# Optimization experiments

Hardware: AMD Instinct MI355X
Metric: run time of the kernel (lower is better)

Reference implementation:

```python
import jax, jax.numpy as jnp
import numpy as np

ND, NT, B = 16384, 16384, 4096
FD, FT, C = 256, 256, 768


def _gat(x_src, x_dst, ei, Ws, Wd, a_s, a_d, b, num_dst, self_loops):
    """PyG GATConv, heads=1: per-edge attention softmax over incoming edges."""
    if self_loops:
        loops = jnp.arange(num_dst, dtype=ei.dtype)
        ei = jnp.concatenate([ei, jnp.stack([loops, loops])], axis=1)
    src, dst = ei[0], ei[1]
    hs = x_src @ Ws                                   # [Ns, C]
    hd = x_dst @ Wd                                   # [Ndst, C]
    e = jax.nn.leaky_relu((hs @ a_s)[src] + (hd @ a_d)[dst], 0.2)   # [E]
    m = jax.ops.segment_max(e, dst, num_segments=num_dst)
    p = jnp.exp(e - m[dst])
    s = jax.ops.segment_sum(p, dst, num_segments=num_dst)
    alpha = p / (s[dst] + 1e-16)
    out = jax.ops.segment_sum(hs[src] * alpha[:, None], dst, num_segments=num_dst)
    return out + b


def _l2norm(x):
    n = jnp.linalg.norm(x, axis=1, keepdims=True)
    return x / jnp.maximum(n, 1e-12)


def setup_inputs() -> dict:
    ks = iter(jax.random.split(jax.random.key(0), 64))
    def nrm(shape, fan_in=None):
        s = 1.0 if fan_in is None else (1.0 / fan_in) ** 0.5
        return jax.random.normal(next(ks), shape, jnp.float32) * s
    inp = {}
    inp["x_drug"] = nrm((ND, FD))
    inp["x_target"] = nrm((NT, FT))
    inp["cell_features"] = nrm((B, 890))
    for et, fs, fd in (("dd", FD, FD), ("dt", FD, FT), ("tt", FT, FT)):
        inp[f"W_src_{et}"] = nrm((fs, C), fs)
        inp[f"W_dst_{et}"] = nrm((fd, C), fd)
        inp[f"a_src_{et}"] = nrm((C,), C)
        inp[f"a_dst_{et}"] = nrm((C,), C)
        inp[f"b_{et}"] = jnp.zeros((C,), jnp.float32)
    for name, fi, fo in (("red1", 890, 2048), ("red2", 2048, 512), ("red3", 512, 2 * C),
                         ("r2a", 4 * C, 2048), ("r2b", 2048, 512), ("r2c", 512, C), ("cls", C, 2)):
        inp[f"{name}_w"] = nrm((fi, fo), fi)
        inp[f"{name}_b"] = jnp.zeros((fo,), jnp.float32)
    inp["drug1_id"] = jax.random.randint(next(ks), (B,), 0, ND)
    inp["drug2_id"] = jax.random.randint(next(ks), (B,), 0, ND)
    inp["ei_dd"] = jax.random.randint(next(ks), (2, 131072), 0, ND)
    inp["ei_dt"] = jnp.stack([jax.random.randint(next(ks), (262144,), 0, ND),
                              jax.random.randint(next(ks), (262144,), 0, NT)])
    inp["ei_tt"] = jax.random.randint(next(ks), (2, 262144), 0, NT)
    return inp


def reference(x_drug, x_target, cell_features,
              W_src_dd, W_dst_dd, a_src_dd, a_dst_dd, b_dd,
              W_src_dt, W_dst_dt, a_src_dt, a_dst_dt, b_dt,
              W_src_tt, W_dst_tt, a_src_tt, a_dst_tt, b_tt,
              red1_w, red1_b, red2_w, red2_b, red3_w, red3_b,
              r2a_w, r2a_b, r2b_w, r2b_b, r2c_w, r2c_b,
              cls_w, cls_b,
              drug1_id, drug2_id, ei_dd, ei_dt, ei_tt):
    # HeteroConv (aggr='sum') followed by per-type ReLU, num_layers=1
    drug = jax.nn.relu(_gat(x_drug, x_drug, ei_dd,
                            W_src_dd, W_dst_dd, a_src_dd, a_dst_dd, b_dd, ND, True))
    target = jax.nn.relu(
        _gat(x_drug, x_target, ei_dt, W_src_dt, W_dst_dt, a_src_dt, a_dst_dt, b_dt, NT, False)
        + _gat(x_target, x_target, ei_tt, W_src_tt, W_dst_tt, a_src_tt, a_dst_tt, b_tt, NT, True))
    del target  # with num_layers=1 the target embeddings never feed the output (faithful)
    d1 = drug[drug1_id]
    d2 = drug[drug2_id]
    cell = _l2norm(cell_features)
    cell = jax.nn.relu(cell @ red1_w + red1_b)
    cell = jax.nn.relu(cell @ red2_w + red2_b)
    cell = jax.nn.relu(cell @ red3_w + red3_b)          # [B, 2*C]
    hidden = _l2norm(jnp.concatenate([d1, d2, cell], axis=1))  # [B, 4*C]
    hidden = jax.nn.relu(hidden @ r2a_w + r2a_b)
    hidden = jax.nn.relu(hidden @ r2b_w + r2b_b)
    hidden = jax.nn.relu(hidden @ r2c_w + r2c_b)
    return hidden @ cls_w + cls_b                       # [B, 2]
```

## Files before the change

kernel.cpp:

```cpp
#include <hip/hip_runtime.h>
#include <cstdint>

#define ND 16384
#define BATCH 4096
#define CDIM 768
#define E_DD 131072
#define FD 256

typedef unsigned short u16;
typedef u16 u16x4 __attribute__((ext_vector_type(4)));
typedef u16 u16x8 __attribute__((ext_vector_type(8)));
typedef short s16x8 __attribute__((ext_vector_type(8)));
typedef float f32x4 __attribute__((ext_vector_type(4)));

__device__ __forceinline__ u16 f2bf(float x) {
  union { float f; uint32_t u; } v; v.f = x;
  uint32_t r = v.u + 0x7fffu + ((v.u >> 16) & 1u);
  return (u16)(r >> 16);
}
__device__ __forceinline__ float bf2f(u16 h) {
  union { float f; uint32_t u; } v; v.u = ((uint32_t)h) << 16;
  return v.f;
}
__device__ __forceinline__ uint32_t split2p(float x) {
  u16 h = f2bf(x);
  u16 l = f2bf(x - bf2f(h));
  return ((uint32_t)h << 16) | l;
}

#define KP 40

template <int KS, int OUT_BF16, int RELU, int BIAS, int ASPLIT, int ALO, int BLO>
__global__ __launch_bounds__(256) void mfma_gemm(
    const float* __restrict__ Af,
    const u16* __restrict__ Ahi, const u16* __restrict__ Alo,
    const u16* __restrict__ Bhi, const u16* __restrict__ Blo,
    const float* __restrict__ bias,
    float* __restrict__ Cf, u16* __restrict__ Chi,
    int M, int N, int K) {
  constexpr int MT = 4, NT = 4;
  constexpr int BM = 128, BN = 128;
  constexpr int ASEG = BM / 64;
  constexpr int BSEG = BN / 64;
  constexpr int AARR = ALO ? 2 : 1;
  constexpr int BARR = BLO ? 2 : 1;
  __shared__ __align__(16) u16 As[AARR][BM][KP];
  __shared__ __align__(16) u16 Bs[BARR][BN][KP];

  const int t = threadIdx.x;
  const int bm0 = blockIdx.x * BM, bn0 = blockIdx.y * BN;
  const int wid = t >> 6, lane = t & 63;
  const int quad = lane >> 4, l16 = lane & 15;
  const int wm0 = (wid >> 1) * (MT * 16);
  const int wn0 = (wid & 1) * (NT * 16);

  const int chunk = K / KS;
  const int kbeg = (KS > 1) ? (int)blockIdx.z * chunk : 0;
  const int kend = kbeg + chunk;

  f32x4 acc[MT][NT];
#pragma unroll
  for (int i = 0; i < MT; ++i)
#pragma unroll
    for (int j = 0; j < NT; ++j) acc[i][j] = (f32x4){0.f, 0.f, 0.f, 0.f};

  u16x8 pAh[ASEG], pAl[ASEG], pBh[BSEG], pBl[BSEG];

  auto loadA = [&](int c, int kk) {
    int s = t + 256 * c, row = s >> 2, kq = (s & 3) * 8;
    size_t off = (size_t)(bm0 + row) * K + kk + kq;
    if (ASPLIT) {
      f32x4 v0 = *(const f32x4*)(Af + off);
      f32x4 v1 = *(const f32x4*)(Af + off + 4);
      u16x8 h, l;
#pragma unroll
      for (int e = 0; e < 4; ++e) {
        uint32_t p = split2p(v0[e]);
        h[e] = (u16)(p >> 16); l[e] = (u16)(p & 0xffffu);
        uint32_t q = split2p(v1[e]);
        h[e + 4] = (u16)(q >> 16); l[e + 4] = (u16)(q & 0xffffu);
      }
      pAh[c] = h; pAl[c] = l;
    } else {
      pAh[c] = *(const u16x8*)(Ahi + off);
      if (ALO) pAl[c] = *(const u16x8*)(Alo + off);
    }
  };
  auto loadB = [&](int c, int kk) {
    int s = t + 256 * c, row = s >> 2, kq = (s & 3) * 8;
    size_t off = (size_t)(bn0 + row) * K + kk + kq;
    pBh[c] = *(const u16x8*)(Bhi + off);
    if (BLO) pBl[c] = *(const u16x8*)(Blo + off);
  };

#pragma unroll
  for (int c = 0; c < ASEG; ++c) loadA(c, kbeg);
#pragma unroll
  for (int c = 0; c < BSEG; ++c) loadB(c, kbeg);

  for (int k0 = kbeg;;) {
    __syncthreads();
#pragma unroll
    for (int c = 0; c < ASEG; ++c) {
      int s = t + 256 * c, row = s >> 2, kq = (s & 3) * 8;
      *(u16x8*)&As[0][row][kq] = pAh[c];
      if (ALO) *(u16x8*)&As[AARR - 1][row][kq] = pAl[c];
    }
#pragma unroll
    for (int c = 0; c < BSEG; ++c) {
      int s = t + 256 * c, row = s >> 2, kq = (s & 3) * 8;
      *(u16x8*)&Bs[0][row][kq] = pBh[c];
      if (BLO) *(u16x8*)&Bs[BARR - 1][row][kq] = pBl[c];
    }
    __syncthreads();

    int kn = k0 + 32;
    if (kn < kend) {
#pragma unroll
      for (int c = 0; c < ASEG; ++c) loadA(c, kn);
#pragma unroll
      for (int c = 0; c < BSEG; ++c) loadB(c, kn);
    }

    s16x8 ah[MT], al[MT], bh[NT], bl[NT];
#pragma unroll
    for (int mi = 0; mi < MT; ++mi) {
      ah[mi] = *(const s16x8*)&As[0][wm0 + mi * 16 + l16][quad * 8];
      if (ALO) al[mi] = *(const s16x8*)&As[AARR - 1][wm0 + mi * 16 + l16][quad * 8];
    }
#pragma unroll
    for (int ni = 0; ni < NT; ++ni) {
      bh[ni] = *(const s16x8*)&Bs[0][wn0 + ni * 16 + l16][quad * 8];
      if (BLO) bl[ni] = *(const s16x8*)&Bs[BARR - 1][wn0 + ni * 16 + l16][quad * 8];
    }
#pragma unroll
    for (int mi = 0; mi < MT; ++mi)
#pragma unroll
      for (int ni = 0; ni < NT; ++ni) {
        acc[mi][ni] = __builtin_amdgcn_mfma_f32_16x16x32_bf16(
            ah[mi], bh[ni], acc[mi][ni], 0, 0, 0);
        if (BLO)
          acc[mi][ni] = __builtin_amdgcn_mfma_f32_16x16x32_bf16(
              ah[mi], bl[ni], acc[mi][ni], 0, 0, 0);
        if (ALO)
          acc[mi][ni] = __builtin_amdgcn_mfma_f32_16x16x32_bf16(
              al[mi], bh[ni], acc[mi][ni], 0, 0, 0);
      }
    k0 = kn;
    if (k0 >= kend) break;
  }

  float* Cp = (KS > 1) ? Cf + (size_t)blockIdx.z * M * N : Cf;
#pragma unroll
  for (int mi = 0; mi < MT; ++mi) {
#pragma unroll
    for (int ni = 0; ni < NT; ++ni) {
      int row = bm0 + wm0 + mi * 16 + quad * 4;
      int col = bn0 + wn0 + ni * 16 + l16;
      float bv = BIAS ? bias[col] : 0.f;
#pragma unroll
      for (int r = 0; r < 4; ++r) {
        float v = acc[mi][ni][r] + bv;
        if (RELU) v = fmaxf(v, 0.f);
        size_t o = (size_t)(row + r) * N + col;
        if (OUT_BF16) {
          Chi[o] = f2bf(v);
        } else {
          Cp[o] = v;
        }
      }
    }
  }
}

template <int KS>
__global__ void reduce_split_ks(const float* __restrict__ P,
                                const float* __restrict__ bias,
                                u16* __restrict__ Chi, int M, int N) {
  int i = blockIdx.x * 256 + threadIdx.x;
  int total = (M * N) >> 2;
  if (i >= total) return;
  f32x4 s = ((const f32x4*)P)[i];
#pragma unroll
  for (int z = 1; z < KS; ++z) s += ((const f32x4*)P)[(size_t)z * total + i];
  int col = (i * 4) % N;
  f32x4 bv = *(const f32x4*)(bias + col);
  u16x4 h;
#pragma unroll
  for (int e = 0; e < 4; ++e) h[e] = f2bf(fmaxf(s[e] + bv[e], 0.f));
  *(u16x4*)&Chi[i * 4] = h;
}

__global__ void reduce_cls(const float* __restrict__ P,
                           const float* __restrict__ bias,
                           const float* __restrict__ clsw,
                           const float* __restrict__ clsb,
                           float* __restrict__ out) {
  int row = blockIdx.x * 4 + (threadIdx.x >> 6);
  int lane = threadIdx.x & 63;
  const f32x4* p0 = (const f32x4*)(P + (size_t)row * CDIM);
  const f32x4* p1 = (const f32x4*)(P + (size_t)BATCH * CDIM + (size_t)row * CDIM);
  float s0 = 0.f, s1 = 0.f;
#pragma unroll
  for (int i = 0; i < 3; ++i) {
    int c4 = lane + 64 * i;
    f32x4 a = p0[c4] + p1[c4];
    f32x4 bv = *(const f32x4*)(bias + c4 * 4);
#pragma unroll
    for (int e = 0; e < 4; ++e) {
      float h = fmaxf(a[e] + bv[e], 0.f);
      int c = c4 * 4 + e;
      s0 = fmaf(h, clsw[c * 2 + 0], s0);
      s1 = fmaf(h, clsw[c * 2 + 1], s1);
    }
  }
#pragma unroll
  for (int m = 32; m; m >>= 1) {
    s0 += __shfl_xor(s0, m);
    s1 += __shfl_xor(s1, m);
  }
  if (lane == 0) {
    out[row * 2 + 0] = s0 + clsb[0];
    out[row * 2 + 1] = s1 + clsb[1];
  }
}

struct TDesc {
  const float* W;
  u16* Th;
  int K, N, Kpad, start;
};
struct TPack { TDesc d[7]; };

__global__ void multi_transpose(TPack p) {
  __shared__ float tile[32][33];
  int b = blockIdx.x;
  int mi = 0;
#pragma unroll
  for (int i = 1; i < 7; ++i)
    if (b >= p.d[i].start) mi = i;
  TDesc dd = p.d[mi];
  int rel = b - dd.start;
  int tilesX = dd.Kpad / 32;
  int k0 = (rel % tilesX) * 32, n0 = (rel / tilesX) * 32;
  int tx = threadIdx.x, ty = threadIdx.y;
#pragma unroll
  for (int i = 0; i < 4; ++i) {
    int k = k0 + ty + 8 * i, n = n0 + tx;
    tile[ty + 8 * i][tx] = (k < dd.K && n < dd.N) ? dd.W[(size_t)k * dd.N + n] : 0.f;
  }
  __syncthreads();
#pragma unroll
  for (int i = 0; i < 4; ++i) {
    int n = n0 + ty + 8 * i, k = k0 + tx;
    if (n < dd.N) dd.Th[(size_t)n * dd.Kpad + k] = f2bf(tile[tx][ty + 8 * i]);
  }
}

__global__ void wvec_kernel(const float* __restrict__ Wsrc,
                            const float* __restrict__ Wdst,
                            const float* __restrict__ a_s,
                            const float* __restrict__ a_d,
                            float* __restrict__ wsv, float* __restrict__ wdv) {
  int k = blockIdx.x;
  int t = threadIdx.x;
  __shared__ float rs[256], rd[256];
  float s = 0.f, d = 0.f;
  for (int c = t; c < CDIM; c += 256) {
    s += Wsrc[(size_t)k * CDIM + c] * a_s[c];
    d += Wdst[(size_t)k * CDIM + c] * a_d[c];
  }
  rs[t] = s; rd[t] = d;
  __syncthreads();
  for (int st = 128; st; st >>= 1) {
    if (t < st) { rs[t] += rs[t + st]; rd[t] += rd[t + st]; }
    __syncthreads();
  }
  if (t == 0) { wsv[k] = rs[0]; wdv[k] = rd[0]; }
}

__global__ void esed_kernel(const float* __restrict__ x,
                            const float* __restrict__ wsv,
                            const float* __restrict__ wdv,
                            float* __restrict__ es, float* __restrict__ ed) {
  int i = blockIdx.x * 256 + threadIdx.x;
  int lane = threadIdx.x & 63;
  int row = i >> 6;
  int c4 = lane * 4;
  f32x4 v = ((const f32x4*)x)[i];
  f32x4 ws = *(const f32x4*)(wsv + c4);
  f32x4 wd = *(const f32x4*)(wdv + c4);
  float a = v[0] * ws[0] + v[1] * ws[1] + v[2] * ws[2] + v[3] * ws[3];
  float b = v[0] * wd[0] + v[1] * wd[1] + v[2] * wd[2] + v[3] * wd[3];
#pragma unroll
  for (int m = 32; m; m >>= 1) {
    a += __shfl_xor(a, m);
    b += __shfl_xor(b, m);
  }
  if (lane == 0) { es[row] = a; ed[row] = b; }
}

__global__ void init_csr(int* counts, int* mask, int* cnt) {
  int i = blockIdx.x * 256 + threadIdx.x;
  if (i < ND) { counts[i] = 1; mask[i] = 0; }
  if (i == 0) *cnt = 0;
}
__global__ void mark_kernel(const int* __restrict__ d1, const int* __restrict__ d2,
                            int* mask) {
  int i = blockIdx.x * 256 + threadIdx.x;
  if (i < BATCH) {
    mask[d1[i]] = 1;
    mask[d2[i]] = 1;
  }
}
__global__ void compact_kernel(const int* __restrict__ mask, int* cnt, int* list) {
  int i = blockIdx.x * 256 + threadIdx.x;
  if (i < ND && mask[i]) {
    int pos = atomicAdd(cnt, 1);
    list[pos] = i;
  }
}

__global__ void count_edges(const int* __restrict__ dst, int* counts) {
  int e = blockIdx.x * 256 + threadIdx.x;
  if (e < E_DD) atomicAdd(&counts[dst[e]], 1);
}
__global__ void scan_kernel(const int* __restrict__ counts, int* __restrict__ offsets,
                            int* __restrict__ cursor, int* __restrict__ slots) {
  __shared__ int part[512];
  int t = threadIdx.x;
  int base = t * 32;
  int s = 0;
  for (int i = 0; i < 32; ++i) s += counts[base + i];
  part[t] = s;
  __syncthreads();
  if (t == 0) {
    int run = 0;
    for (int i = 0; i < 512; ++i) { int tmp = part[i]; part[i] = run; run += tmp; }
    offsets[ND] = run;
  }
  __syncthreads();
  int run = part[t];
  for (int i = 0; i < 32; ++i) {
    int d = base + i;
    offsets[d] = run;
    slots[run] = d;
    cursor[d] = run + 1;
    run += counts[d];
  }
}
__global__ void scatter_edges(const int* __restrict__ src, const int* __restrict__ dst,
                              int* cursor, int* slots) {
  int e = blockIdx.x * 256 + threadIdx.x;
  if (e < E_DD) {
    int pos = atomicAdd(&cursor[dst[e]], 1);
    slots[pos] = src[e];
  }
}

__global__ __launch_bounds__(256) void gat_aggregate(
    const u16* __restrict__ hs, const float* __restrict__ es,
    const float* __restrict__ ed, const int* __restrict__ offsets,
    const int* __restrict__ slots, const float* __restrict__ bias,
    const int* __restrict__ list, const int* __restrict__ cnt,
    u16* __restrict__ out) {
  int idx = blockIdx.x * 4 + (threadIdx.x >> 6);
  if (idx >= *cnt) return;
  int d = list[idx];
  int lane = threadIdx.x & 63;
  int beg = offsets[d], end = offsets[d + 1];
  float edv = ed[d];
  float mx = -1e30f;
  for (int j = beg + lane; j < end; j += 64) {
    float e = es[slots[j]] + edv;
    e = e >= 0.f ? e : 0.2f * e;
    mx = fmaxf(mx, e);
  }
#pragma unroll
  for (int m = 32; m; m >>= 1) mx = fmaxf(mx, __shfl_xor(mx, m));
  float sm = 0.f;
  for (int j = beg + lane; j < end; j += 64) {
    float e = es[slots[j]] + edv;
    e = e >= 0.f ? e : 0.2f * e;
    sm += expf(e - mx);
  }
#pragma unroll
  for (int m = 32; m; m >>= 1) sm += __shfl_xor(sm, m);
  float inv = 1.f / (sm + 1e-16f);
  f32x4 a0 = {0.f, 0.f, 0.f, 0.f}, a1 = a0, a2 = a0;
  int c4 = lane * 4;
  for (int j = beg; j < end; ++j) {
    int srcn = slots[j];
    float e = es[srcn] + edv;
    e = e >= 0.f ? e : 0.2f * e;
    float alpha = expf(e - mx) * inv;
    const u16* hrow = hs + (size_t)srcn * CDIM;
    u16x4 r0 = *(const u16x4*)(hrow + c4);
    u16x4 r1 = *(const u16x4*)(hrow + 256 + c4);
    u16x4 r2 = *(const u16x4*)(hrow + 512 + c4);
#pragma unroll
    for (int e2 = 0; e2 < 4; ++e2) {
      a0[e2] = fmaf(alpha, bf2f(r0[e2]), a0[e2]);
      a1[e2] = fmaf(alpha, bf2f(r1[e2]), a1[e2]);
      a2[e2] = fmaf(alpha, bf2f(r2[e2]), a2[e2]);
    }
  }
  u16* orow = out + (size_t)d * CDIM;
  u16x4 o0, o1, o2;
#pragma unroll
  for (int e2 = 0; e2 < 4; ++e2) {
    o0[e2] = f2bf(fmaxf(a0[e2] + bias[c4 + e2], 0.f));
    o1[e2] = f2bf(fmaxf(a1[e2] + bias[256 + c4 + e2], 0.f));
    o2[e2] = f2bf(fmaxf(a2[e2] + bias[512 + c4 + e2], 0.f));
  }
  *(u16x4*)(orow + c4) = o0;
  *(u16x4*)(orow + 256 + c4) = o1;
  *(u16x4*)(orow + 512 + c4) = o2;
}

__global__ void l2norm_bf16(const float* __restrict__ in, u16* __restrict__ hi,
                            int L, int Lp) {
  int row = blockIdx.x;
  int t = threadIdx.x;
  __shared__ float red[256];
  const float* irow = in + (size_t)row * L;
  float s = 0.f;
  for (int c = t; c < L; c += 256) { float v = irow[c]; s += v * v; }
  red[t] = s;
  __syncthreads();
  for (int st = 128; st; st >>= 1) {
    if (t < st) red[t] += red[t + st];
    __syncthreads();
  }
  float inv = 1.f / fmaxf(sqrtf(red[0]), 1e-12f);
  for (int c = t; c < Lp; c += 256) {
    float v = (c < L) ? irow[c] * inv : 0.f;
    hi[(size_t)row * Lp + c] = f2bf(v);
  }
}

__global__ __launch_bounds__(256) void hidden_build_bf16(
    const u16* __restrict__ drug, const u16* __restrict__ c3,
    const int* __restrict__ d1, const int* __restrict__ d2,
    u16* __restrict__ hhi) {
  int row = blockIdx.x;
  int t = threadIdx.x;
  const u16* s1 = drug + (size_t)d1[row] * CDIM;
  const u16* s2 = drug + (size_t)d2[row] * CDIM;
  const u16* s3 = c3 + (size_t)row * (2 * CDIM);
  float vals[12];
  float ss = 0.f;
#pragma unroll
  for (int i = 0; i < 12; ++i) {
    int c = t + 256 * i;
    float v;
    if (i < 3)      v = bf2f(s1[c]);
    else if (i < 6) v = bf2f(s2[c - CDIM]);
    else            v = bf2f(s3[c - 2 * CDIM]);
    vals[i] = v;
    ss += v * v;
  }
  __shared__ float red[256];
  red[t] = ss;
  __syncthreads();
  for (int st = 128; st; st >>= 1) {
    if (t < st) red[t] += red[t + st];
    __syncthreads();
  }
  float inv = 1.f / fmaxf(sqrtf(red[0]), 1e-12f);
  u16* hrow_h = hhi + (size_t)row * (4 * CDIM);
#pragma unroll
  for (int i = 0; i < 12; ++i) hrow_h[t + 256 * i] = f2bf(vals[i] * inv);
}

extern "C" void kernel_launch(void* const* d_in, const int* in_sizes, int n_in,
                              void* d_out, int out_size, void* d_ws, size_t ws_size,
                              hipStream_t stream) {
  const float* x_drug   = (const float*)d_in[0];
  const float* cellf    = (const float*)d_in[2];
  const float* W_src_dd = (const float*)d_in[3];
  const float* W_dst_dd = (const float*)d_in[4];
  const float* a_src_dd = (const float*)d_in[5];
  const float* a_dst_dd = (const float*)d_in[6];
  const float* b_dd     = (const float*)d_in[7];
  const float* red1_w = (const float*)d_in[18];
  const float* red1_b = (const float*)d_in[19];
  const float* red2_w = (const float*)d_in[20];
  const float* red2_b = (const float*)d_in[21];
  const float* red3_w = (const float*)d_in[22];
  const float* red3_b = (const float*)d_in[23];
  const float* r2a_w  = (const float*)d_in[24];
  const float* r2a_b  = (const float*)d_in[25];
  const float* r2b_w  = (const float*)d_in[26];
  const float* r2b_b  = (const float*)d_in[27];
  const float* r2c_w  = (const float*)d_in[28];
  const float* r2c_b  = (const float*)d_in[29];
  const float* cls_w  = (const float*)d_in[30];
  const float* cls_b  = (const float*)d_in[31];
  const int* drug1_id = (const int*)d_in[32];
  const int* drug2_id = (const int*)d_in[33];
  const int* ei_dd    = (const int*)d_in[34];
  float* out = (float*)d_out;

  const int* dd_src = ei_dd;
  const int* dd_dst = ei_dd + E_DD;

  char* w = (char*)d_ws;
  size_t off = 0;
  auto alloc = [&](size_t bytes) -> char* {
    char* p = w + off;
    off = (off + bytes + 255) & ~(size_t)255;
    return p;
  };
  u16* hs   = (u16*)alloc((size_t)ND * CDIM * 2);
  u16* drug = (u16*)alloc((size_t)ND * CDIM * 2);
  u16* c3   = (u16*)alloc((size_t)BATCH * 2 * CDIM * 2);
  float* P  = (float*)alloc((size_t)4 * BATCH * 512 * 4);
  u16* hid_hi = hs;
  u16* cn_hi = (u16*)alloc((size_t)BATCH * 896 * 2);
  u16* c1_hi = (u16*)alloc((size_t)BATCH * 2048 * 2);
  u16* c2_hi = (u16*)alloc((size_t)BATCH * 512 * 2);
  u16* wsrcT_hi = (u16*)alloc((size_t)CDIM * FD * 2);
  u16* r1T_hi = (u16*)alloc((size_t)2048 * 896 * 2);
  u16* r2T_hi = (u16*)alloc((size_t)512 * 2048 * 2);
  u16* r3T_hi = (u16*)alloc((size_t)1536 * 512 * 2);
  u16* raT_hi = (u16*)alloc((size_t)2048 * 3072 * 2);
  u16* rbT_hi = (u16*)alloc((size_t)512 * 2048 * 2);
  u16* rcT_hi = (u16*)alloc((size_t)768 * 512 * 2);
  float* es  = (float*)alloc((size_t)ND * 4);
  float* ed  = (float*)alloc((size_t)ND * 4);
  float* wsv = (float*)alloc(FD * 4);
  float* wdv = (float*)alloc(FD * 4);
  int* counts  = (int*)alloc((size_t)ND * 4);
  int* offsets = (int*)alloc((size_t)(ND + 1) * 4);
  int* cursor  = (int*)alloc((size_t)ND * 4);
  int* slots   = (int*)alloc((size_t)(E_DD + ND) * 4);
  int* mask    = (int*)alloc((size_t)ND * 4);
  int* list    = (int*)alloc((size_t)ND * 4);
  int* cnt     = (int*)alloc(256);
  (void)ws_size; (void)n_in; (void)in_sizes; (void)out_size;

  TPack tp;
  tp.d[0] = {W_src_dd, wsrcT_hi, 256, 768, 256, 0};
  tp.d[1] = {red1_w, r1T_hi, 890, 2048, 896, 192};
  tp.d[2] = {red2_w, r2T_hi, 2048, 512, 2048, 1984};
  tp.d[3] = {red3_w, r3T_hi, 512, 1536, 512, 3008};
  tp.d[4] = {r2a_w, raT_hi, 3072, 2048, 3072, 3776};
  tp.d[5] = {r2b_w, rbT_hi, 2048, 512, 2048, 9920};
  tp.d[6] = {r2c_w, rcT_hi, 512, 768, 512, 10944};
  multi_transpose<<<11328, dim3(32, 8), 0, stream>>>(tp);

  wvec_kernel<<<FD, 256, 0, stream>>>(W_src_dd, W_dst_dd, a_src_dd, a_dst_dd, wsv, wdv);
  esed_kernel<<<ND * FD / 1024, 256, 0, stream>>>(x_drug, wsv, wdv, es, ed);
  init_csr<<<ND / 256, 256, 0, stream>>>(counts, mask, cnt);
  mark_kernel<<<BATCH / 256, 256, 0, stream>>>(drug1_id, drug2_id, mask);
  compact_kernel<<<ND / 256, 256, 0, stream>>>(mask, cnt, list);

  l2norm_bf16<<<BATCH, 256, 0, stream>>>(cellf, cn_hi, 890, 896);
  mfma_gemm<1, 1, 1, 1, 0, 0, 0><<<dim3(BATCH / 128, 2048 / 128), 256, 0, stream>>>(
      nullptr, cn_hi, nullptr, r1T_hi, nullptr, red1_b, nullptr, c1_hi, BATCH, 2048, 896);
  mfma_gemm<4, 0, 0, 0, 0, 0, 0><<<dim3(BATCH / 128, 512 / 128, 4), 256, 0, stream>>>(
      nullptr, c1_hi, nullptr, r2T_hi, nullptr, nullptr, P, nullptr, BATCH, 512, 2048);
  reduce_split_ks<4><<<BATCH * 512 / 1024, 256, 0, stream>>>(P, red2_b, c2_hi, BATCH, 512);
  mfma_gemm<1, 1, 1, 1, 0, 0, 0><<<dim3(BATCH / 128, 1536 / 128), 256, 0, stream>>>(
      nullptr, c2_hi, nullptr, r3T_hi, nullptr, red3_b, nullptr, c3, BATCH, 1536, 512);

  mfma_gemm<1, 1, 0, 0, 1, 1, 0><<<dim3(ND / 128, CDIM / 128), 256, 0, stream>>>(
      x_drug, nullptr, nullptr, wsrcT_hi, nullptr, nullptr, nullptr, hs, ND, CDIM, FD);
  count_edges<<<E_DD / 256, 256, 0, stream>>>(dd_dst, counts);
  scan_kernel<<<1, 512, 0, stream>>>(counts, offsets, cursor, slots);
  scatter_edges<<<E_DD / 256, 256, 0, stream>>>(dd_src, dd_dst, cursor, slots);
  gat_aggregate<<<ND / 4, 256, 0, stream>>>(hs, es, ed, offsets, slots, b_dd, list, cnt, drug);

  hidden_build_bf16<<<BATCH, 256, 0, stream>>>(drug, c3, drug1_id, drug2_id, hid_hi);

  mfma_gemm<1, 1, 1, 1, 0, 0, 0><<<dim3(BATCH / 128, 2048 / 128), 256, 0, stream>>>(
      nullptr, hid_hi, nullptr, raT_hi, nullptr, r2a_b, nullptr, c1_hi, BATCH, 2048, 3072);
  mfma_gemm<4, 0, 0, 0, 0, 0, 0><<<dim3(BATCH / 128, 512 / 128, 4), 256, 0, stream>>>(
      nullptr, c1_hi, nullptr, rbT_hi, nullptr, nullptr, P, nullptr, BATCH, 512, 2048);
  reduce_split_ks<4><<<BATCH * 512 / 1024, 256, 0, stream>>>(P, r2b_b, c2_hi, BATCH, 512);
  mfma_gemm<2, 0, 0, 0, 0, 0, 0><<<dim3(BATCH / 128, CDIM / 128, 2), 256, 0, stream>>>(
      nullptr, c2_hi, nullptr, rcT_hi, nullptr, nullptr, P, nullptr, BATCH, CDIM, 512);
  reduce_cls<<<BATCH / 4, 256, 0, stream>>>(P, r2c_b, cls_w, cls_b, out);
}
```

Before: 491.9 us.

## Merge red1 and hs GEMMs into one launch; widen GAT aggregate loads

Refactors the GEMM body into a device function taking block indices and shared-memory pointers, then launches the red1 cell GEMM (512 tiles) and the x_drug→hs GEMM (768 tiles) together as a single 1280-block kernel. This removes one launch and lets two independent, smaller grids fill the GPU concurrently. The shared buffers are sized for the larger (split-A) variant, which may lower occupancy for the red1 tiles. The GAT aggregation also switches to one 16-byte load plus one 8-byte load per row instead of three 8-byte loads.

Result: faster. 479.6 us (-2.5%).

```diff
diff --git a/kernel.cpp b/kernel.cpp
--- a/kernel.cpp
+++ b/kernel.cpp
@@ -31,32 +31,32 @@
 #define KP 40
 
 template <int KS, int OUT_BF16, int RELU, int BIAS, int ASPLIT, int ALO, int BLO>
-__global__ __launch_bounds__(256) void mfma_gemm(
+__device__ __forceinline__ void gemm_core(
+    int bx, int by, int bz,
     const float* __restrict__ Af,
     const u16* __restrict__ Ahi, const u16* __restrict__ Alo,
     const u16* __restrict__ Bhi, const u16* __restrict__ Blo,
     const float* __restrict__ bias,
     float* __restrict__ Cf, u16* __restrict__ Chi,
-    int M, int N, int K) {
+    int M, int N, int K, u16* AsB, u16* BsB) {
   constexpr int MT = 4, NT = 4;
   constexpr int BM = 128, BN = 128;
   constexpr int ASEG = BM / 64;
   constexpr int BSEG = BN / 64;
-  constexpr int AARR = ALO ? 2 : 1;
-  constexpr int BARR = BLO ? 2 : 1;
-  __shared__ __align__(16) u16 As[AARR][BM][KP];
-  __shared__ __align__(16) u16 Bs[BARR][BN][KP];
 
   const int t = threadIdx.x;
-  const int bm0 = blockIdx.x * BM, bn0 = blockIdx.y * BN;
+  const int bm0 = bx * BM, bn0 = by * BN;
   const int wid = t >> 6, lane = t & 63;
   const int quad = lane >> 4, l16 = lane & 15;
   const int wm0 = (wid >> 1) * (MT * 16);
   const int wn0 = (wid & 1) * (NT * 16);
 
   const int chunk = K / KS;
-  const int kbeg = (KS > 1) ? (int)blockIdx.z * chunk : 0;
+  const int kbeg = (KS > 1) ? bz * chunk : 0;
   const int kend = kbeg + chunk;
+
+  auto As = [&](int a, int r, int k) -> u16& { return AsB[(a * BM + r) * KP + k]; };
+  auto Bs = [&](int a, int r, int k) -> u16& { return BsB[(a * BN + r) * KP + k]; };
 
   f32x4 acc[MT][NT];
 #pragma unroll
@@ -103,14 +103,14 @@
 #pragma unroll
     for (int c = 0; c < ASEG; ++c) {
       int s = t + 256 * c, row = s >> 2, kq = (s & 3) * 8;
-      *(u16x8*)&As[0][row][kq] = pAh[c];
-      if (ALO) *(u16x8*)&As[AARR - 1][row][kq] = pAl[c];
+      *(u16x8*)&As(0, row, kq) = pAh[c];
+      if (ALO) *(u16x8*)&As(1, row, kq) = pAl[c];
     }
 #pragma unroll
     for (int c = 0; c < BSEG; ++c) {
       int s = t + 256 * c, row = s >> 2, kq = (s & 3) * 8;
-      *(u16x8*)&Bs[0][row][kq] = pBh[c];
-      if (BLO) *(u16x8*)&Bs[BARR - 1][row][kq] = pBl[c];
+      *(u16x8*)&Bs(0, row, kq) = pBh[c];
+      if (BLO) *(u16x8*)&Bs(1, row, kq) = pBl[c];
     }
     __syncthreads();
 
@@ -125,13 +125,13 @@
     s16x8 ah[MT], al[MT], bh[NT], bl[NT];
 #pragma unroll
     for (int mi = 0; mi < MT; ++mi) {
-      ah[mi] = *(const s16x8*)&As[0][wm0 + mi * 16 + l16][quad * 8];
-      if (ALO) al[mi] = *(const s16x8*)&As[AARR - 1][wm0 + mi * 16 + l16][quad * 8];
+      ah[mi] = *(const s16x8*)&As(0, wm0 + mi * 16 + l16, quad * 8);
+      if (ALO) al[mi] = *(const s16x8*)&As(1, wm0 + mi * 16 + l16, quad * 8);
     }
 #pragma unroll
     for (int ni = 0; ni < NT; ++ni) {
-      bh[ni] = *(const s16x8*)&Bs[0][wn0 + ni * 16 + l16][quad * 8];
-      if (BLO) bl[ni] = *(const s16x8*)&Bs[BARR - 1][wn0 + ni * 16 + l16][quad * 8];
+      bh[ni] = *(const s16x8*)&Bs(0, wn0 + ni * 16 + l16, quad * 8);
+      if (BLO) bl[ni] = *(const s16x8*)&Bs(1, wn0 + ni * 16 + l16, quad * 8);
     }
 #pragma unroll
     for (int mi = 0; mi < MT; ++mi)
@@ -150,7 +150,7 @@
     if (k0 >= kend) break;
   }
 
-  float* Cp = (KS > 1) ? Cf + (size_t)blockIdx.z * M * N : Cf;
+  float* Cp = (KS > 1) ? Cf + (size_t)bz * M * N : Cf;
 #pragma unroll
   for (int mi = 0; mi < MT; ++mi) {
 #pragma unroll
@@ -163,13 +163,45 @@
         float v = acc[mi][ni][r] + bv;
         if (RELU) v = fmaxf(v, 0.f);
         size_t o = (size_t)(row + r) * N + col;
-        if (OUT_BF16) {
-          Chi[o] = f2bf(v);
-        } else {
-          Cp[o] = v;
-        }
+        if (OUT_BF16) Chi[o] = f2bf(v);
+        else Cp[o] = v;
       }
     }
+  }
+}
+
+template <int KS, int OUT_BF16, int RELU, int BIAS, int ASPLIT, int ALO, int BLO>
+__global__ __launch_bounds__(256) void mfma_gemm(
+    const float* __restrict__ Af,
+    const u16* __restrict__ Ahi, const u16* __restrict__ Alo,
+    const u16* __restrict__ Bhi, const u16* __restrict__ Blo,
+    const float* __restrict__ bias,
+    float* __restrict__ Cf, u16* __restrict__ Chi,
+    int M, int N, int K) {
+  __shared__ __align__(16) u16 AsB[(ALO ? 2 : 1) * 128 * KP];
+  __shared__ __align__(16) u16 BsB[(BLO ? 2 : 1) * 128 * KP];
+  gemm_core<KS, OUT_BF16, RELU, BIAS, ASPLIT, ALO, BLO>(
+      blockIdx.x, blockIdx.y, (KS > 1) ? (int)blockIdx.z : 0,
+      Af, Ahi, Alo, Bhi, Blo, bias, Cf, Chi, M, N, K, AsB, BsB);
+}
+
+__global__ __launch_bounds__(256) void dual_gemm_red1_hs(
+    const u16* __restrict__ cn, const u16* __restrict__ r1T,
+    const float* __restrict__ red1_b, u16* __restrict__ c1,
+    const float* __restrict__ xd, const u16* __restrict__ wsrcT,
+    u16* __restrict__ hs) {
+  __shared__ __align__(16) u16 AsB[2 * 128 * KP];
+  __shared__ __align__(16) u16 BsB[128 * KP];
+  int b = blockIdx.x;
+  if (b < 512) {
+    gemm_core<1, 1, 1, 1, 0, 0, 0>(b & 31, b >> 5, 0, nullptr, cn, nullptr,
+                                   r1T, nullptr, red1_b, nullptr, c1,
+                                   BATCH, 2048, 896, AsB, BsB);
+  } else {
+    int b2 = b - 512;
+    gemm_core<1, 1, 0, 0, 1, 1, 0>(b2 & 127, b2 >> 7, 0, xd, nullptr, nullptr,
+                                   wsrcT, nullptr, nullptr, nullptr, hs,
+                                   ND, CDIM, FD, AsB, BsB);
   }
 }
 
@@ -387,35 +419,32 @@
 #pragma unroll
   for (int m = 32; m; m >>= 1) sm += __shfl_xor(sm, m);
   float inv = 1.f / (sm + 1e-16f);
-  f32x4 a0 = {0.f, 0.f, 0.f, 0.f}, a1 = a0, a2 = a0;
-  int c4 = lane * 4;
+  int c8 = lane * 8;
+  int c4 = 512 + lane * 4;
+  float a8[8] = {};
+  float a4[4] = {};
   for (int j = beg; j < end; ++j) {
     int srcn = slots[j];
     float e = es[srcn] + edv;
     e = e >= 0.f ? e : 0.2f * e;
     float alpha = expf(e - mx) * inv;
     const u16* hrow = hs + (size_t)srcn * CDIM;
-    u16x4 r0 = *(const u16x4*)(hrow + c4);
-    u16x4 r1 = *(const u16x4*)(hrow + 256 + c4);
-    u16x4 r2 = *(const u16x4*)(hrow + 512 + c4);
-#pragma unroll
-    for (int e2 = 0; e2 < 4; ++e2) {
-      a0[e2] = fmaf(alpha, bf2f(r0[e2]), a0[e2]);
-      a1[e2] = fmaf(alpha, bf2f(r1[e2]), a1[e2]);
-      a2[e2] = fmaf(alpha, bf2f(r2[e2]), a2[e2]);
-    }
+    u16x8 r8 = *(const u16x8*)(hrow + c8);
+    u16x4 r4 = *(const u16x4*)(hrow + c4);
+#pragma unroll
+    for (int e2 = 0; e2 < 8; ++e2) a8[e2] = fmaf(alpha, bf2f(r8[e2]), a8[e2]);
+#pragma unroll
+    for (int e2 = 0; e2 < 4; ++e2) a4[e2] = fmaf(alpha, bf2f(r4[e2]), a4[e2]);
   }
   u16* orow = out + (size_t)d * CDIM;
-  u16x4 o0, o1, o2;
-#pragma unroll
-  for (int e2 = 0; e2 < 4; ++e2) {
-    o0[e2] = f2bf(fmaxf(a0[e2] + bias[c4 + e2], 0.f));
-    o1[e2] = f2bf(fmaxf(a1[e2] + bias[256 + c4 + e2], 0.f));
-    o2[e2] = f2bf(fmaxf(a2[e2] + bias[512 + c4 + e2], 0.f));
-  }
-  *(u16x4*)(orow + c4) = o0;
-  *(u16x4*)(orow + 256 + c4) = o1;
-  *(u16x4*)(orow + 512 + c4) = o2;
+  u16x8 o8;
+  u16x4 o4;
+#pragma unroll
+  for (int e2 = 0; e2 < 8; ++e2) o8[e2] = f2bf(fmaxf(a8[e2] + bias[c8 + e2], 0.f));
+#pragma unroll
+  for (int e2 = 0; e2 < 4; ++e2) o4[e2] = f2bf(fmaxf(a4[e2] + bias[c4 + e2], 0.f));
+  *(u16x8*)(orow + c8) = o8;
+  *(u16x4*)(orow + c4) = o4;
 }
 
 __global__ void l2norm_bf16(const float* __restrict__ in, u16* __restrict__ hi,
@@ -555,18 +584,17 @@
   init_csr<<<ND / 256, 256, 0, stream>>>(counts, mask, cnt);
   mark_kernel<<<BATCH / 256, 256, 0, stream>>>(drug1_id, drug2_id, mask);
   compact_kernel<<<ND / 256, 256, 0, stream>>>(mask, cnt, list);
-
   l2norm_bf16<<<BATCH, 256, 0, stream>>>(cellf, cn_hi, 890, 896);
-  mfma_gemm<1, 1, 1, 1, 0, 0, 0><<<dim3(BATCH / 128, 2048 / 128), 256, 0, stream>>>(
-      nullptr, cn_hi, nullptr, r1T_hi, nullptr, red1_b, nullptr, c1_hi, BATCH, 2048, 896);
+
+  dual_gemm_red1_hs<<<1280, 256, 0, stream>>>(cn_hi, r1T_hi, red1_b, c1_hi,
+                                              x_drug, wsrcT_hi, hs);
+
   mfma_gemm<4, 0, 0, 0, 0, 0, 0><<<dim3(BATCH / 128, 512 / 128, 4), 256, 0, stream>>>(
       nullptr, c1_hi, nullptr, r2T_hi, nullptr, nullptr, P, nullptr, BATCH, 512, 2048);
   reduce_split_ks<4><<<BATCH * 512 / 1024, 256, 0, stream>>>(P, red2_b, c2_hi, BATCH, 512);
   mfma_gemm<1, 1, 1, 1, 0, 0, 0><<<dim3(BATCH / 128, 1536 / 128), 256, 0, stream>>>(
       nullptr, c2_hi, nullptr, r3T_hi, nullptr, red3_b, nullptr, c3, BATCH, 1536, 512);
 
-  mfma_gemm<1, 1, 0, 0, 1, 1, 0><<<dim3(ND / 128, CDIM / 128), 256, 0, stream>>>(
-      x_drug, nullptr, nullptr, wsrcT_hi, nullptr, nullptr, nullptr, hs, ND, CDIM, FD);
   count_edges<<<E_DD / 256, 256, 0, stream>>>(dd_dst, counts);
   scan_kernel<<<1, 512, 0, stream>>>(counts, offsets, cursor, slots);
   scatter_edges<<<E_DD / 256, 256, 0, stream>>>(dd_src, dd_dst, cursor, slots);
```
